# Performance work log

Measured on AMD Instinct MI355X. Metric: run time of the kernel, lower is better.

Reference implementation:

```python
import jax, jax.numpy as jnp
import numpy as np

N = 30000
DEG = 16
E_RAND = N * DEG
E = E_RAND + N  # with self loops appended
T = 2
F_IN, H1, OUT = 128, 128, 64
NBSZ = 15
AGG = 0.8
NEG_SLOPE = 0.2


def setup_inputs() -> dict:
    key = jax.random.key(0)
    ks = jax.random.split(key, 10)
    x_all = jax.random.normal(ks[0], (T, N, F_IN), dtype=jnp.float32)
    # edges per snapshot: random edges + self loops (mirrors remove_self_loops + add_self_loops)
    loops = jnp.arange(N, dtype=jnp.int32)
    eis = []
    for t in range(T):
        src = jax.random.randint(jax.random.fold_in(ks[1], t), (E_RAND,), 0, N, dtype=jnp.int32)
        dst = jax.random.randint(jax.random.fold_in(ks[2], t), (E_RAND,), 0, N, dtype=jnp.int32)
        eis.append(jnp.stack([jnp.concatenate([src, loops]), jnp.concatenate([dst, loops])]))
    edge_index_all = jnp.stack(eis)  # [T, 2, E]
    def glorot(k, shape):
        fan = shape[0] + shape[-1]
        s = jnp.sqrt(6.0 / fan)
        return jax.random.uniform(k, shape, jnp.float32, -s, s)
    W1 = glorot(ks[3], (F_IN, 2 * H1))
    att1 = glorot(ks[4], (1, 1, 4 * H1))   # [1, heads=1, 2*out_neurons]
    b1 = jnp.zeros((2 * H1,), jnp.float32)
    W2 = glorot(ks[5], (H1, 2 * OUT))
    att2 = glorot(ks[6], (1, 1, 4 * OUT))
    b2 = jnp.zeros((2 * OUT,), jnp.float32)
    return {"x_all": x_all, "edge_index_all": edge_index_all,
            "W1": W1, "att1": att1, "b1": b1, "W2": W2, "att2": att2, "b2": b2}


def _conv(x, edge_index, W, att, b, C):
    """One DGIBConv (heads=1, Bernoulli distribution, diag reparam, eval mode).
    Returns (node_out [N,C], ixz scalar, structure_kl scalar)."""
    h = x @ W                                    # [N, 2C]
    src, dst = edge_index[0], edge_index[1]
    x_j = h[src]                                 # [E, 2C] per-edge gather (source)
    x_i = h[dst]                                 # [E, 2C] target
    a = att[0, 0]                                # [4C]
    logits = jnp.sum(x_i * a[:2 * C], -1) + jnp.sum(x_j * a[2 * C:], -1)  # [E]
    logits = jax.nn.leaky_relu(logits, NEG_SLOPE)
    # Bernoulli branch: softmax of ones over segments == 1/deg(dst)
    deg = jax.ops.segment_sum(jnp.ones_like(logits), dst, num_segments=N)  # [N]
    norm = 1.0 / deg[dst]
    p = jnp.clip(jax.nn.sigmoid(logits), 0.01, 0.99)  # posterior Bernoulli probs
    alpha = p * norm
    aggr = jax.ops.segment_sum(x_j * alpha[:, None], dst, num_segments=N) + b  # [N, 2C]
    # diag reparam: mean || std-logit split; Gaussian prior N(0, I)
    mu = aggr[:, :C]
    std = jax.nn.softplus(aggr[:, C:]) + 1e-10
    kl = -jnp.log(std) + 0.5 * (std * std + mu * mu) - 0.5  # KL(N(mu,std)||N(0,1)) per dim
    ixz = jnp.mean(jnp.sum(kl, -1))
    # structure KL: Bernoulli(p) || Bernoulli(logits = 1/nbsz)
    q = jax.nn.sigmoid(jnp.float32(1.0 / NBSZ))
    skl = jnp.mean(p * jnp.log(p / q) + (1.0 - p) * jnp.log((1.0 - p) / (1.0 - q)))
    return mu, ixz, skl


def _layer(x_list, edge_index_all, W, att, b, C):
    """Temporal DGIBConv.forward: per-snapshot conv + weighted temporal fusion."""
    outs, ixzs, skls = [], [], []
    for t in range(T):
        out, ixz, skl = _conv(x_list[t], edge_index_all[t], W, att, b, C)
        if t > 0:
            w = jax.nn.sigmoid(jnp.arange(t, dtype=jnp.float32))[:, None, None]  # [t,1,1]
            prev = jnp.stack(outs[:t])                                           # [t,N,C]
            out = jnp.sum(w * prev, 0) / t * AGG + out * (1.0 - AGG)
        outs.append(out)
        ixzs.append(ixz)
        skls.append(skl)
    return outs, jnp.mean(jnp.stack(ixzs)), jnp.mean(jnp.stack(skls))


def reference(x_all, edge_index_all, W1, att1, b1, W2, att2, b2):
    xs = [x_all[t] for t in range(T)]
    h1, ixz1, skl1 = _layer(xs, edge_index_all, W1, att1, b1, H1)
    h1 = [jax.nn.relu(h) for h in h1]  # with_relu=True, eval -> dropout is identity
    h2, ixz2, skl2 = _layer(h1, edge_index_all, W2, att2, b2, OUT)
    out = jnp.stack(h2)                # [T, N, OUT]
    ixz_mean = (ixz1 + ixz2) / 2.0
    skl_mean = (skl1 + skl2) / 2.0
    return out, ixz_mean, skl_mean
```

## Files before the change

### kernel.cpp

```cpp
#include <hip/hip_runtime.h>
#include <hip/hip_bf16.h>

#define N_NODES 30000
#define N_EDGES 510000
#define K_DIM   128
#define ABLK    7500

typedef short bf16x8 __attribute__((ext_vector_type(8)));
typedef float f32x4  __attribute__((ext_vector_type(4)));
typedef float f32x2  __attribute__((ext_vector_type(2)));
typedef unsigned int u32x2 __attribute__((ext_vector_type(2)));

__device__ __forceinline__ unsigned short f2bf(float f) {
  __hip_bfloat16 h = __float2bfloat16(f);
  return *(unsigned short*)&h;
}

__global__ void prep_kernel(const float* __restrict__ W1, unsigned short* __restrict__ Wt1,
                            const float* __restrict__ W2, unsigned short* __restrict__ Wt2,
                            const int* __restrict__ ei, int* __restrict__ deg0,
                            int* __restrict__ deg1, int e) {
  int i = blockIdx.x * blockDim.x + threadIdx.x;
  if (i < 128 * 256) {
    int k = i >> 8, m = i & 255;
    Wt1[m * 128 + k] = f2bf(W1[i]);
  } else if (i < 128 * 256 + 128 * 128) {
    int j = i - 128 * 256;
    int k = j >> 7, m = j & 127;
    Wt2[m * 128 + k] = f2bf(W2[j]);
  }
  if (i < 2 * e) {
    int t = i >= e ? 1 : 0;
    int j = i - t * e;
    int d = ei[(size_t)t * 2 * e + e + j];
    atomicAdd(&(t ? deg1 : deg0)[d], 1);
  }
}

__global__ __launch_bounds__(1024) void scan_kernel(const int* __restrict__ deg0, int* __restrict__ off0,
                                                    int* __restrict__ cur0, float* __restrict__ rn0,
                                                    const int* __restrict__ deg1, int* __restrict__ off1,
                                                    int* __restrict__ cur1, float* __restrict__ rn1,
                                                    int n) {
  const int* deg = blockIdx.x ? deg1 : deg0;
  int* off = blockIdx.x ? off1 : off0;
  int* cur = blockIdx.x ? cur1 : cur0;
  float* rn = blockIdx.x ? rn1 : rn0;
  const int CHUNK = 30;
  __shared__ int wsum[16];
  int tid = threadIdx.x;
  int base = tid * CHUNK;
  int sum = 0;
  for (int i = 0; i < CHUNK; i++)
    if (base + i < n) sum += deg[base + i];
  int lane = tid & 63, wid = tid >> 6;
  int incl = sum;
#pragma unroll
  for (int o = 1; o < 64; o <<= 1) {
    int v = __shfl_up(incl, o);
    if (lane >= o) incl += v;
  }
  if (lane == 63) wsum[wid] = incl;
  __syncthreads();
  if (tid == 0) {
    int run = 0;
    for (int w = 0; w < 16; w++) { int v = wsum[w]; wsum[w] = run; run += v; }
  }
  __syncthreads();
  int run = incl - sum + wsum[wid];
  for (int i = 0; i < CHUNK; i++) {
    if (base + i < n) {
      int dg = deg[base + i];
      off[base + i] = run;
      cur[base + i] = run;
      rn[base + i] = 1.0f / (float)dg;
      run += dg;
    }
  }
}

__global__ void scatter_kernel(const int* __restrict__ ei,
                               int* __restrict__ cur0, int* __restrict__ cur1,
                               unsigned int* __restrict__ csr0, unsigned int* __restrict__ csr1, int e) {
  int i = blockIdx.x * blockDim.x + threadIdx.x;
  if (i < 2 * e) {
    int t = i >= e ? 1 : 0;
    int j = i - t * e;
    int s = ei[(size_t)t * 2 * e + j];
    int d = ei[(size_t)t * 2 * e + e + j];
    int* cur = t ? cur1 : cur0;
    unsigned int* csr = t ? csr1 : csr0;
    int p = atomicAdd(&cur[d], 1);
    csr[p] = (unsigned int)s | ((unsigned int)d << 16);
  }
}

template<int M, int MODE>
__global__ __launch_bounds__(256) void gemm_kernel(const void* __restrict__ X0v,
                                                   const void* __restrict__ X1v,
                                                   const short* __restrict__ Wt,
                                                   unsigned char* __restrict__ H0,
                                                   unsigned char* __restrict__ H1,
                                                   const float* __restrict__ att,
                                                   float* __restrict__ si0, float* __restrict__ si1,
                                                   float* __restrict__ sj0, float* __restrict__ sj1,
                                                   int nrows) {
  int t = blockIdx.y;
  unsigned char* Hf8 = t ? H1 : H0;
  float* s_i = t ? si1 : si0;
  float* s_j = t ? sj1 : sj0;

  int wave = blockIdx.x * 4 + (threadIdx.x >> 6);
  int lane = threadIdx.x & 63;
  if (wave * 16 >= nrows) return;
  int m16 = lane & 15, quad = lane >> 4;

  bf16x8 a[4];
  size_t arow = (size_t)(wave * 16 + m16) * K_DIM + quad * 8;
  if constexpr (MODE == 0) {
    const float* X = (const float*)(t ? X1v : X0v);
#pragma unroll
    for (int kc = 0; kc < 4; kc++) {
      f32x4 lo = *(const f32x4*)(X + arow + kc * 32);
      f32x4 hi = *(const f32x4*)(X + arow + kc * 32 + 4);
#pragma unroll
      for (int j = 0; j < 4; j++) {
        ((unsigned short*)&a[kc])[j]     = f2bf(lo[j]);
        ((unsigned short*)&a[kc])[4 + j] = f2bf(hi[j]);
      }
    }
  } else {
    const float* Xa = (const float*)X0v;
    const float* Xb = (const float*)X1v;
#pragma unroll
    for (int kc = 0; kc < 4; kc++) {
      f32x4 lo = *(const f32x4*)(Xa + arow + kc * 32);
      f32x4 hi = *(const f32x4*)(Xa + arow + kc * 32 + 4);
      if (t) {
        f32x4 lo1 = *(const f32x4*)(Xb + arow + kc * 32);
        f32x4 hi1 = *(const f32x4*)(Xb + arow + kc * 32 + 4);
        lo = lo * 0.4f + lo1 * 0.2f;
        hi = hi * 0.4f + hi1 * 0.2f;
      }
#pragma unroll
      for (int j = 0; j < 4; j++) {
        ((unsigned short*)&a[kc])[j]     = f2bf(fmaxf(lo[j], 0.f));
        ((unsigned short*)&a[kc])[4 + j] = f2bf(fmaxf(hi[j], 0.f));
      }
    }
  }

  float sip[4] = {0.f, 0.f, 0.f, 0.f}, sjp[4] = {0.f, 0.f, 0.f, 0.f};
#pragma unroll
  for (int nt = 0; nt < M / 16; nt++) {
    f32x4 acc = {0.f, 0.f, 0.f, 0.f};
    size_t brow = (size_t)(nt * 16 + m16) * K_DIM + quad * 8;
#pragma unroll
    for (int kc = 0; kc < 4; kc++) {
      bf16x8 b = *(const bf16x8*)(Wt + brow + kc * 32);
      acc = __builtin_amdgcn_mfma_f32_16x16x32_bf16(a[kc], b, acc, 0, 0, 0);
    }
    int col = nt * 16 + m16;
    float aA = att[col], aB = att[M + col];
#pragma unroll
    for (int r = 0; r < 4; r++) {
      int row = wave * 16 + quad * 4 + r;
      int pk = __builtin_amdgcn_cvt_pk_fp8_f32(acc[r], acc[r], 0, false);
      Hf8[(size_t)row * M + col] = (unsigned char)pk;
      sip[r] += acc[r] * aA;
      sjp[r] += acc[r] * aB;
    }
  }
#pragma unroll
  for (int o = 1; o < 16; o <<= 1) {
#pragma unroll
    for (int r = 0; r < 4; r++) {
      sip[r] += __shfl_xor(sip[r], o);
      sjp[r] += __shfl_xor(sjp[r], o);
    }
  }
  if (m16 == 0) {
#pragma unroll
    for (int r = 0; r < 4; r++) {
      int row = wave * 16 + quad * 4 + r;
      s_i[row] = sip[r];
      s_j[row] = sjp[r];
    }
  }
}

template<int M>
__global__ __launch_bounds__(256) void aggr_kernel(const unsigned char* __restrict__ H0,
                                                   const unsigned char* __restrict__ H1,
                                                   const unsigned int* __restrict__ csr0,
                                                   const unsigned int* __restrict__ csr1,
                                                   const int* __restrict__ off0, const int* __restrict__ off1,
                                                   const int* __restrict__ deg0, const int* __restrict__ deg1,
                                                   const float* __restrict__ rn0, const float* __restrict__ rn1,
                                                   const float* __restrict__ si0, const float* __restrict__ si1,
                                                   const float* __restrict__ sj0, const float* __restrict__ sj1,
                                                   const float* __restrict__ bias,
                                                   float* __restrict__ mu0, float* __restrict__ mu1,
                                                   f32x2* __restrict__ part,
                                                   int n) {
  constexpr int C = M / 2;
  constexpr int LPR = M / 8;
  constexpr int L2LPR = (M == 256) ? 5 : 4;
  constexpr int EPL = 64 / LPR;
  constexpr int NL = 4;
  constexpr int U = NL * EPL;

  int t = blockIdx.y;
  const unsigned char* Hf8 = t ? H1 : H0;
  const unsigned int* csr = t ? csr1 : csr0;
  const int* off = t ? off1 : off0;
  const int* deg = t ? deg1 : deg0;
  const float* rn = t ? rn1 : rn0;
  const float* s_i = t ? si1 : si0;
  const float* s_j = t ? sj1 : sj0;
  float* mu = t ? mu1 : mu0;

  __shared__ f32x2 red[4];
  int wid = threadIdx.x >> 6, lane = threadIdx.x & 63;
  int wave = blockIdx.x * 4 + wid;
  float ixz = 0.f, skl = 0.f;

  if (wave < n) {
    int d     = __builtin_amdgcn_readfirstlane(deg[wave]);
    int start = __builtin_amdgcn_readfirstlane(off[wave]);
    float siv = s_i[wave];
    float rnv = rn[wave];
    int sub = lane & (LPR - 1);
    int g   = lane >> L2LPR;
    const unsigned char* hbase = Hf8 + sub * 8;

    const float qc  = 1.0f / (1.0f + __expf(-(1.0f / 15.0f)));
    const float lq  = __logf(qc);
    const float l1q = __logf(1.0f - qc);

    f32x2 acc[4];
#pragma unroll
    for (int k = 0; k < 4; k++) acc[k] = {0.f, 0.f};

    for (int base = 0; base < d; base += 64) {
      int ee = base + lane;
      unsigned int ce = csr[start + (ee < d ? ee : d - 1)];
      int src = (int)(ce & 0xffffu);
      float sj = s_j[src];
      float lg = siv + sj;
      lg = lg > 0.f ? lg : 0.2f * lg;
      float pv = 1.0f / (1.0f + __expf(-lg));
      pv = fminf(fmaxf(pv, 0.01f), 0.99f);
      if (ee < d)
        skl += pv * (__logf(pv) - lq) + (1.0f - pv) * (__logf(1.0f - pv) - l1q);
      float wval = (ee < d) ? pv * rnv : 0.f;

      int cnt = min(d - base, 64);
      for (int c0 = 0; c0 < cnt; c0 += U) {
        int srcl[NL];
        float wl[NL];
#pragma unroll
        for (int l = 0; l < NL; l++) {
          int idx = c0 + l * EPL + g;
          srcl[l] = __shfl(src, idx);
          wl[l]   = __shfl(wval, idx);
        }
        u32x2 hv[NL];
#pragma unroll
        for (int l = 0; l < NL; l++)
          hv[l] = *(const u32x2*)(hbase + (size_t)srcl[l] * M);
#pragma unroll
        for (int l = 0; l < NL; l++) {
          f32x2 wv = {wl[l], wl[l]};
          f32x2 d0 = __builtin_amdgcn_cvt_pk_f32_fp8((int)hv[l][0], false);
          f32x2 d1 = __builtin_amdgcn_cvt_pk_f32_fp8((int)hv[l][0], true);
          f32x2 d2 = __builtin_amdgcn_cvt_pk_f32_fp8((int)hv[l][1], false);
          f32x2 d3 = __builtin_amdgcn_cvt_pk_f32_fp8((int)hv[l][1], true);
          acc[0] = d0 * wv + acc[0];
          acc[1] = d1 * wv + acc[1];
          acc[2] = d2 * wv + acc[2];
          acc[3] = d3 * wv + acc[3];
        }
      }
    }

#pragma unroll
    for (int o = LPR; o < 64; o <<= 1) {
#pragma unroll
      for (int j = 0; j < 4; j++) {
        acc[j][0] += __shfl_xor(acc[j][0], o);
        acc[j][1] += __shfl_xor(acc[j][1], o);
      }
    }

    if (lane < LPR) {
      int ch0 = sub * 8;
      if (ch0 < C) {
        f32x4 mv[2];
#pragma unroll
        for (int j = 0; j < 4; j++) {
          float a0 = acc[j][0] + bias[ch0 + 2 * j];
          float a1 = acc[j][1] + bias[ch0 + 2 * j + 1];
          ixz += 0.5f * (a0 * a0 + a1 * a1) - 1.0f;
          mv[j >> 1][(j & 1) * 2]     = a0;
          mv[j >> 1][(j & 1) * 2 + 1] = a1;
        }
        *(f32x4*)(mu + (size_t)wave * C + ch0)     = mv[0];
        *(f32x4*)(mu + (size_t)wave * C + ch0 + 4) = mv[1];
      } else {
#pragma unroll
        for (int j = 0; j < 4; j++) {
#pragma unroll
          for (int h = 0; h < 2; h++) {
            float a = acc[j][h] + bias[ch0 + 2 * j + h];
            float sp = (a > 20.f) ? a : log1pf(__expf(a));
            sp += 1e-10f;
            ixz += -__logf(sp) + 0.5f * sp * sp;
          }
        }
      }
    }
  }
#pragma unroll
  for (int o = 32; o > 0; o >>= 1) {
    ixz += __shfl_xor(ixz, o);
    skl += __shfl_xor(skl, o);
  }
  if (lane == 0) { f32x2 r; r[0] = ixz; r[1] = skl; red[wid] = r; }
  __syncthreads();
  if (threadIdx.x == 0) {
    f32x2 pr = red[0] + red[1] + red[2] + red[3];
    part[t * ABLK + blockIdx.x] = pr;
  }
}

__global__ void fuse2_kernel(const float* __restrict__ mu0, const float* __restrict__ mu1,
                             float* __restrict__ out, int n) {
  int i = blockIdx.x * blockDim.x + threadIdx.x;
  if (i < n) {
    float m0 = mu0[i], m1 = mu1[i];
    out[i] = m0;
    out[n + i] = 0.4f * m0 + 0.2f * m1;
  }
}

__global__ __launch_bounds__(1024) void reduce_kernel(const f32x2* __restrict__ p1,
                                                      const f32x2* __restrict__ p2,
                                                      float* __restrict__ out2) {
  __shared__ float ri[16], rs[16];
  float ixz = 0.f, skl = 0.f;
  for (int i = threadIdx.x; i < 2 * ABLK; i += 1024) {
    f32x2 a = p1[i], b = p2[i];
    ixz += a[0] + b[0];
    skl += a[1] + b[1];
  }
  int lane = threadIdx.x & 63, wid = threadIdx.x >> 6;
#pragma unroll
  for (int o = 32; o > 0; o >>= 1) {
    ixz += __shfl_xor(ixz, o);
    skl += __shfl_xor(skl, o);
  }
  if (lane == 0) { ri[wid] = ixz; rs[wid] = skl; }
  __syncthreads();
  if (threadIdx.x == 0) {
    float si = 0.f, ss = 0.f;
    for (int w = 0; w < 16; w++) { si += ri[w]; ss += rs[w]; }
    out2[0] = si / (4.0f * (float)N_NODES);
    out2[1] = ss / (4.0f * (float)N_EDGES);
  }
}

extern "C" void kernel_launch(void* const* d_in, const int* in_sizes, int n_in,
                              void* d_out, int out_size, void* d_ws, size_t ws_size,
                              hipStream_t stream) {
  const float* x_all = (const float*)d_in[0];
  const int* ei      = (const int*)d_in[1];
  const float* W1    = (const float*)d_in[2];
  const float* att1  = (const float*)d_in[3];
  const float* b1    = (const float*)d_in[4];
  const float* W2    = (const float*)d_in[5];
  const float* att2  = (const float*)d_in[6];
  const float* b2    = (const float*)d_in[7];
  float* out         = (float*)d_out;

  char* ws = (char*)d_ws;
  size_t off = 0;
  auto alloc = [&](size_t bytes) {
    char* p = ws + off;
    off = (off + bytes + 255) & ~(size_t)255;
    return p;
  };
  unsigned short* wt1  = (unsigned short*)alloc(256 * 128 * sizeof(short));
  unsigned short* wt2  = (unsigned short*)alloc(128 * 128 * sizeof(short));
  unsigned char* hf8_0 = (unsigned char*)alloc((size_t)N_NODES * 256);
  unsigned char* hf8_1 = (unsigned char*)alloc((size_t)N_NODES * 256);
  float* si0   = (float*)alloc(N_NODES * sizeof(float));
  float* si1   = (float*)alloc(N_NODES * sizeof(float));
  float* sj0   = (float*)alloc(N_NODES * sizeof(float));
  float* sj1   = (float*)alloc(N_NODES * sizeof(float));
  float* mu1_0 = (float*)alloc((size_t)N_NODES * 128 * sizeof(float));
  float* mu1_1 = (float*)alloc((size_t)N_NODES * 128 * sizeof(float));
  float* mu2_0 = mu1_0;
  float* mu2_1 = mu1_0 + (size_t)N_NODES * 64;
  int* degbase  = (int*)alloc(2 * N_NODES * 4);
  int* degp[2]  = {degbase, degbase + N_NODES};
  int* offp[2]  = {(int*)alloc(N_NODES * 4), (int*)alloc(N_NODES * 4)};
  int* curp[2]  = {(int*)alloc(N_NODES * 4), (int*)alloc(N_NODES * 4)};
  float* rnp[2] = {(float*)alloc(N_NODES * 4), (float*)alloc(N_NODES * 4)};
  unsigned int* csrp[2] = {(unsigned int*)alloc((size_t)N_EDGES * 4),
                           (unsigned int*)alloc((size_t)N_EDGES * 4)};
  f32x2* part1 = (f32x2*)alloc(2 * ABLK * sizeof(f32x2));
  f32x2* part2 = (f32x2*)alloc(2 * ABLK * sizeof(f32x2));

  hipMemsetAsync(degbase, 0, 2 * N_NODES * 4, stream);

  prep_kernel<<<(2 * N_EDGES + 255) / 256, 256, 0, stream>>>(W1, wt1, W2, wt2,
                                                             ei, degp[0], degp[1], N_EDGES);
  scan_kernel<<<2, 1024, 0, stream>>>(degp[0], offp[0], curp[0], rnp[0],
                                      degp[1], offp[1], curp[1], rnp[1], N_NODES);
  scatter_kernel<<<(2 * N_EDGES + 255) / 256, 256, 0, stream>>>(ei, curp[0], curp[1],
                                                                csrp[0], csrp[1], N_EDGES);

  dim3 ggrid(469, 2), agrid(ABLK, 2);

  const float* x0 = x_all;
  const float* x1 = x_all + (size_t)N_NODES * K_DIM;
  gemm_kernel<256, 0><<<ggrid, 256, 0, stream>>>(x0, x1, (const short*)wt1, hf8_0, hf8_1,
                                                 att1, si0, si1, sj0, sj1, N_NODES);
  aggr_kernel<256><<<agrid, 256, 0, stream>>>(hf8_0, hf8_1, csrp[0], csrp[1], offp[0], offp[1],
                                              degp[0], degp[1], rnp[0], rnp[1],
                                              si0, si1, sj0, sj1, b1, mu1_0, mu1_1, part1, N_NODES);

  gemm_kernel<128, 1><<<ggrid, 256, 0, stream>>>(mu1_0, mu1_1, (const short*)wt2, hf8_0, hf8_1,
                                                 att2, si0, si1, sj0, sj1, N_NODES);
  aggr_kernel<128><<<agrid, 256, 0, stream>>>(hf8_0, hf8_1, csrp[0], csrp[1], offp[0], offp[1],
                                              degp[0], degp[1], rnp[0], rnp[1],
                                              si0, si1, sj0, sj1, b2, mu2_0, mu2_1, part2, N_NODES);
  fuse2_kernel<<<(N_NODES * 64 + 255) / 256, 256, 0, stream>>>(mu2_0, mu2_1, out, N_NODES * 64);
  reduce_kernel<<<1, 1024, 0, stream>>>(part1, part2, out + (size_t)2 * N_NODES * 64);
}
```

Baseline: 603.2 us.

## Replace single-block degree scan with multi-block three-pass scan; nontemporal gather loads

The degree prefix scan ran on only two 1024-thread blocks, each thread looping serially over 30 strided elements. It is replaced by a three-kernel reduce, scan and write-out pipeline over 59 blocks per snapshot, with coalesced accesses and shared-memory staging. This spreads a serial, poorly coalesced step across the GPU at the cost of two extra kernel launches. Separately, the fp8 feature gathers in the aggregation kernel now use nontemporal loads to reduce cache pollution, which risks losing reuse of rows that are gathered repeatedly.

Measured after the change: 540.0 us. 10.5% less time.

```diff
diff --git a/kernel.cpp b/kernel.cpp
--- a/kernel.cpp
+++ b/kernel.cpp
@@ -5,6 +5,8 @@
 #define N_EDGES 510000
 #define K_DIM   128
 #define ABLK    7500
+#define SB      59
+#define SCHUNK  512
 
 typedef short bf16x8 __attribute__((ext_vector_type(8)));
 typedef float f32x4  __attribute__((ext_vector_type(4)));
@@ -37,46 +39,83 @@
   }
 }
 
-__global__ __launch_bounds__(1024) void scan_kernel(const int* __restrict__ deg0, int* __restrict__ off0,
-                                                    int* __restrict__ cur0, float* __restrict__ rn0,
-                                                    const int* __restrict__ deg1, int* __restrict__ off1,
-                                                    int* __restrict__ cur1, float* __restrict__ rn1,
-                                                    int n) {
-  const int* deg = blockIdx.x ? deg1 : deg0;
-  int* off = blockIdx.x ? off1 : off0;
-  int* cur = blockIdx.x ? cur1 : cur0;
-  float* rn = blockIdx.x ? rn1 : rn0;
-  const int CHUNK = 30;
-  __shared__ int wsum[16];
-  int tid = threadIdx.x;
-  int base = tid * CHUNK;
+__global__ __launch_bounds__(256) void bsum_kernel(const int* __restrict__ deg0, const int* __restrict__ deg1,
+                                                   float* __restrict__ rn0, float* __restrict__ rn1,
+                                                   int* __restrict__ bsums,
+                                                   int n) {
+  int t = blockIdx.y;
+  const int* deg = t ? deg1 : deg0;
+  float* rn = t ? rn1 : rn0;
+  __shared__ int red[4];
+  int base = blockIdx.x * SCHUNK;
   int sum = 0;
-  for (int i = 0; i < CHUNK; i++)
-    if (base + i < n) sum += deg[base + i];
-  int lane = tid & 63, wid = tid >> 6;
-  int incl = sum;
+#pragma unroll
+  for (int r = 0; r < 2; r++) {
+    int idx = base + r * 256 + threadIdx.x;
+    if (idx < n) {
+      int d = deg[idx];
+      sum += d;
+      rn[idx] = 1.0f / (float)d;
+    }
+  }
+  int lane = threadIdx.x & 63, wid = threadIdx.x >> 6;
+#pragma unroll
+  for (int o = 32; o > 0; o >>= 1) sum += __shfl_xor(sum, o);
+  if (lane == 0) red[wid] = sum;
+  __syncthreads();
+  if (threadIdx.x == 0) bsums[t * SB + blockIdx.x] = red[0] + red[1] + red[2] + red[3];
+}
+
+__global__ __launch_bounds__(128) void bscan_kernel(int* __restrict__ bsums) {
+  int wid = threadIdx.x >> 6, lane = threadIdx.x & 63;
+  int v = (lane < SB) ? bsums[wid * SB + lane] : 0;
+  int incl = v;
 #pragma unroll
   for (int o = 1; o < 64; o <<= 1) {
-    int v = __shfl_up(incl, o);
-    if (lane >= o) incl += v;
-  }
-  if (lane == 63) wsum[wid] = incl;
+    int u = __shfl_up(incl, o);
+    if (lane >= o) incl += u;
+  }
+  if (lane < SB) bsums[wid * SB + lane] = incl - v;
+}
+
+__global__ __launch_bounds__(256) void wout_kernel(const int* __restrict__ deg0, const int* __restrict__ deg1,
+                                                   const int* __restrict__ bsums,
+                                                   int* __restrict__ off0, int* __restrict__ cur0,
+                                                   int* __restrict__ off1, int* __restrict__ cur1,
+                                                   int n) {
+  int t = blockIdx.y;
+  const int* deg = t ? deg1 : deg0;
+  int* off = t ? off1 : off0;
+  int* cur = t ? cur1 : cur0;
+  __shared__ int lds[SCHUNK];
+  __shared__ int wpre[4];
+  int base = blockIdx.x * SCHUNK;
+#pragma unroll
+  for (int r = 0; r < 2; r++) {
+    int i = r * 256 + threadIdx.x;
+    int idx = base + i;
+    lds[i] = (idx < n) ? deg[idx] : 0;
+  }
   __syncthreads();
-  if (tid == 0) {
-    int run = 0;
-    for (int w = 0; w < 16; w++) { int v = wsum[w]; wsum[w] = run; run += v; }
-  }
+  int lane = threadIdx.x & 63, wid = threadIdx.x >> 6;
+  int l0 = lds[2 * threadIdx.x], l1 = lds[2 * threadIdx.x + 1];
+  int s = l0 + l1;
+  int incl = s;
+#pragma unroll
+  for (int o = 1; o < 64; o <<= 1) {
+    int u = __shfl_up(incl, o);
+    if (lane >= o) incl += u;
+  }
+  if (lane == 63) wpre[wid] = incl;
   __syncthreads();
-  int run = incl - sum + wsum[wid];
-  for (int i = 0; i < CHUNK; i++) {
-    if (base + i < n) {
-      int dg = deg[base + i];
-      off[base + i] = run;
-      cur[base + i] = run;
-      rn[base + i] = 1.0f / (float)dg;
-      run += dg;
-    }
-  }
+  int wbase = 0;
+  if (wid > 0) wbase = wpre[0];
+  if (wid > 1) wbase += wpre[1];
+  if (wid > 2) wbase += wpre[2];
+  int P = bsums[t * SB + blockIdx.x] + wbase + incl - s;
+  int e0 = base + 2 * threadIdx.x;
+  if (e0 < n)     { off[e0] = P;          cur[e0] = P; }
+  if (e0 + 1 < n) { off[e0 + 1] = P + l0; cur[e0 + 1] = P + l0; }
 }
 
 __global__ void scatter_kernel(const int* __restrict__ ei,
@@ -268,7 +307,7 @@
         u32x2 hv[NL];
 #pragma unroll
         for (int l = 0; l < NL; l++)
-          hv[l] = *(const u32x2*)(hbase + (size_t)srcl[l] * M);
+          hv[l] = __builtin_nontemporal_load((const u32x2*)(hbase + (size_t)srcl[l] * M));
 #pragma unroll
         for (int l = 0; l < NL; l++) {
           f32x2 wv = {wl[l], wl[l]};
@@ -409,6 +448,7 @@
   float* rnp[2] = {(float*)alloc(N_NODES * 4), (float*)alloc(N_NODES * 4)};
   unsigned int* csrp[2] = {(unsigned int*)alloc((size_t)N_EDGES * 4),
                            (unsigned int*)alloc((size_t)N_EDGES * 4)};
+  int* bsums   = (int*)alloc(2 * SB * sizeof(int));
   f32x2* part1 = (f32x2*)alloc(2 * ABLK * sizeof(f32x2));
   f32x2* part2 = (f32x2*)alloc(2 * ABLK * sizeof(f32x2));
 
@@ -416,8 +456,11 @@
 
   prep_kernel<<<(2 * N_EDGES + 255) / 256, 256, 0, stream>>>(W1, wt1, W2, wt2,
                                                              ei, degp[0], degp[1], N_EDGES);
-  scan_kernel<<<2, 1024, 0, stream>>>(degp[0], offp[0], curp[0], rnp[0],
-                                      degp[1], offp[1], curp[1], rnp[1], N_NODES);
+  dim3 sgrid(SB, 2);
+  bsum_kernel<<<sgrid, 256, 0, stream>>>(degp[0], degp[1], rnp[0], rnp[1], bsums, N_NODES);
+  bscan_kernel<<<1, 128, 0, stream>>>(bsums);
+  wout_kernel<<<sgrid, 256, 0, stream>>>(degp[0], degp[1], bsums,
+                                         offp[0], curp[0], offp[1], curp[1], N_NODES);
   scatter_kernel<<<(2 * N_EDGES + 255) / 256, 256, 0, stream>>>(ei, curp[0], curp[1],
                                                                 csrp[0], csrp[1], N_EDGES);
 
```
